# Kernel tuning notes

Measured on AMD Instinct MI355X. Metric: run time of the kernel, lower is better.

The kernel has to match this reference:

```python
import jax, jax.numpy as jnp
import numpy as np

N_NODES = 100000
N_EDGES = 640000
NODE_D = 128   # node_emb_dim == edge_type_emb_dim (required by reverse-net input dim)
MSG_D = 128


def setup_inputs() -> dict:
    key = jax.random.key(0)
    ks = jax.random.split(key, 10)
    cat_d = 3 * NODE_D  # 2*node_emb + edge_type_emb
    s_msg = 1.0 / np.sqrt(cat_d)
    s_upd = 1.0 / np.sqrt(MSG_D)
    return {
        "node_features": jax.random.normal(ks[0], (N_NODES, NODE_D), jnp.float32),
        "edge_features": jax.random.normal(ks[1], (N_EDGES, NODE_D), jnp.float32),
        "from_idx": jax.random.randint(ks[2], (N_EDGES,), 0, N_NODES, jnp.int32),
        "to_idx": jax.random.randint(ks[3], (N_EDGES,), 0, N_NODES, jnp.int32),
        # message net (Linear + ReLU)
        "W_msg": jax.random.uniform(ks[4], (cat_d, MSG_D), jnp.float32, -s_msg, s_msg),
        "b_msg": jnp.zeros((MSG_D,), jnp.float32),
        # reverse message net (separate params)
        "W_rev": jax.random.uniform(ks[5], (cat_d, MSG_D), jnp.float32, -s_msg, s_msg),
        "b_rev": jnp.zeros((MSG_D,), jnp.float32),
        # node-update MLP (Linear + ReLU), residual update
        "W_upd": jax.random.uniform(ks[6], (MSG_D, NODE_D), jnp.float32, -s_upd, s_upd),
        "b_upd": jnp.zeros((NODE_D,), jnp.float32),
    }


def reference(node_features, edge_features, from_idx, to_idx,
              W_msg, b_msg, W_rev, b_rev, W_upd, b_upd):
    # gather endpoints and concat with edge features: [n_edges, 3*node_d]
    edge_inputs = jnp.concatenate(
        [node_features[from_idx], node_features[to_idx], edge_features], axis=-1)
    # forward + reverse message nets (same inputs, different params), summed
    messages = (jax.nn.relu(edge_inputs @ W_msg + b_msg)
                + jax.nn.relu(edge_inputs @ W_rev + b_rev))
    # scatter-sum into destination nodes: [n_nodes, msg_d]
    aggregated = jax.ops.segment_sum(messages, to_idx, num_segments=N_NODES)
    # residual node update: node + MLP(agg)
    return node_features + jax.nn.relu(aggregated @ W_upd + b_upd)
```

## Files before the change

### kernel.cpp

```cpp
#include <hip/hip_runtime.h>
#include <hip/hip_bf16.h>

#define N_NODES 100000
#define N_EDGES 640000

typedef __bf16 bf16_t;
typedef __bf16 bf16x8 __attribute__((ext_vector_type(8)));
typedef float f32x4 __attribute__((ext_vector_type(4)));
typedef float f4 __attribute__((ext_vector_type(4)));
typedef unsigned int u32x4 __attribute__((ext_vector_type(4)));

__device__ __forceinline__ float bflo(unsigned int u) { return __uint_as_float(u << 16); }
__device__ __forceinline__ float bfhi(unsigned int u) { return __uint_as_float(u & 0xffff0000u); }
__device__ __forceinline__ unsigned int bfpack(float a, float b) {
    union { bf16_t h[2]; unsigned int u; } pk;
    pk.h[0] = (bf16_t)a; pk.h[1] = (bf16_t)b;
    return pk.u;
}

__global__ void hist_kernel(const int* __restrict__ to_idx, int* __restrict__ hist) {
    int e = blockIdx.x * 256 + threadIdx.x;
    if (e < N_EDGES) atomicAdd(&hist[to_idx[e]], 1);
}

#define SCAN_CH 1000

__global__ __launch_bounds__(1024)
void scan_reduce_kernel(const int* __restrict__ hist, int* __restrict__ bsum) {
    __shared__ int red[1024];
    int b = blockIdx.x, t = threadIdx.x;
    int v = (t < SCAN_CH) ? hist[b * SCAN_CH + t] : 0;
    red[t] = v;
    __syncthreads();
    for (int off = 512; off > 0; off >>= 1) {
        if (t < off) red[t] += red[t + off];
        __syncthreads();
    }
    if (t == 0) bsum[b] = red[0];
}

__global__ __launch_bounds__(128)
void scan_base_kernel(const int* __restrict__ bsum, int* __restrict__ bbase) {
    __shared__ int s[128];
    int t = threadIdx.x;
    int v = (t < 100) ? bsum[t] : 0;
    s[t] = v;
    __syncthreads();
    for (int off = 1; off < 128; off <<= 1) {
        int u = (t >= off) ? s[t - off] : 0;
        __syncthreads();
        s[t] += u;
        __syncthreads();
    }
    if (t < 100) bbase[t] = s[t] - v;
}

__global__ __launch_bounds__(1024)
void scan_final_kernel(const int* __restrict__ hist,
                       const int* __restrict__ bbase,
                       int* __restrict__ cursor,
                       int* __restrict__ row_start) {
    __shared__ int s[1024];
    int b = blockIdx.x, t = threadIdx.x;
    int v = (t < SCAN_CH) ? hist[b * SCAN_CH + t] : 0;
    s[t] = v;
    __syncthreads();
    for (int off = 1; off < 1024; off <<= 1) {
        int u = (t >= off) ? s[t - off] : 0;
        __syncthreads();
        s[t] += u;
        __syncthreads();
    }
    int excl = bbase[b] + s[t] - v;
    if (t < SCAN_CH) {
        cursor[b * SCAN_CH + t] = excl;
        row_start[b * SCAN_CH + t] = excl;
    }
    if (b == 99 && t == SCAN_CH - 1) row_start[N_NODES] = excl + v;
}

__global__ void inv_scatter_kernel(const int* __restrict__ to_idx,
                                   int* __restrict__ cursor,
                                   int* __restrict__ inv) {
    int e = blockIdx.x * 256 + threadIdx.x;
    if (e < N_EDGES) {
        int pos = atomicAdd(&cursor[to_idx[e]], 1);
        inv[e] = pos;
    }
}

__global__ void prep_w_new(const float* __restrict__ Wmsg,
                           const float* __restrict__ Wrev,
                           const float* __restrict__ Wupd,
                           bf16_t* __restrict__ Wt1,
                           bf16_t* __restrict__ WtE,
                           bf16_t* __restrict__ WtU) {
    int idx = blockIdx.x * 256 + threadIdx.x;
    if (idx < 512 * 128) {
        int p = idx >> 7, k = idx & 127;
        int blk = p >> 7, c = p & 127;
        float v;
        if (blk == 0)      v = Wmsg[k * 128 + c];
        else if (blk == 1) v = Wrev[k * 128 + c];
        else if (blk == 2) v = Wmsg[(128 + k) * 128 + c];
        else               v = Wrev[(128 + k) * 128 + c];
        Wt1[idx] = (bf16_t)v;
    }
    if (idx < 256 * 128) {
        int p = idx >> 7, k = idx & 127;
        float v = (p < 128) ? Wmsg[(256 + k) * 128 + p]
                            : Wrev[(256 + k) * 128 + (p - 128)];
        WtE[idx] = (bf16_t)v;
    }
    if (idx < 128 * 128) {
        int n = idx >> 7, p = idx & 127;
        int colp = 32 * (p >> 5) + ((p >> 1) & 15) + 16 * (p & 1);
        WtU[idx] = (bf16_t)Wupd[colp * 128 + n];
    }
}

__global__ __launch_bounds__(512, 4)
void proj_node_kernel(const float* __restrict__ nodef,
                      const bf16_t* __restrict__ Wt1,
                      unsigned int* __restrict__ A_u) {
    __shared__ char lds_raw[64 * 256];
    const int tid = threadIdx.x;
    const int nb = blockIdx.x * 64;
    const int by = blockIdx.y;

#pragma unroll
    for (int j = 0; j < 4; ++j) {
        int linear = tid + 512 * j;
        int r = linear >> 5, q = linear & 31;
        int node = nb + r;
        f4 v = (f4){0.f, 0.f, 0.f, 0.f};
        if (node < N_NODES)
            v = *reinterpret_cast<const f4*>(nodef + (size_t)node * 128 + q * 4);
        union { bf16_t b[4]; uint2 u; } pk;
        pk.b[0] = (bf16_t)v[0]; pk.b[1] = (bf16_t)v[1];
        pk.b[2] = (bf16_t)v[2]; pk.b[3] = (bf16_t)v[3];
        int byte = (r * 256 + q * 8) ^ ((r & 7) << 4);
        *reinterpret_cast<uint2*>(lds_raw + byte) = pk.u;
    }
    __syncthreads();

    const int wv = tid >> 6;
    const int wr = wv >> 2, wc = wv & 3;
    const int lane = tid & 63;
    const int lhi = lane >> 4, llo = lane & 15;

    f32x4 acc[2][4];
#pragma unroll
    for (int m = 0; m < 2; ++m)
#pragma unroll
        for (int n = 0; n < 4; ++n)
            acc[m][n] = (f32x4){0.f, 0.f, 0.f, 0.f};

    const bf16_t* bptr[4];
#pragma unroll
    for (int n = 0; n < 4; ++n) {
        int colb = (n < 2) ? (wc * 32 + 16 * n) : (128 + wc * 32 + 16 * (n - 2));
        bptr[n] = Wt1 + (size_t)(by * 256 + colb + llo) * 128 + lhi * 8;
    }

#pragma unroll
    for (int k0 = 0; k0 < 4; ++k0) {
        bf16x8 a[2], b[4];
#pragma unroll
        for (int m = 0; m < 2; ++m) {
            int ra = wr * 32 + 16 * m + llo;
            int byte = (ra * 256 + (k0 * 32 + lhi * 8) * 2) ^ ((ra & 7) << 4);
            a[m] = *reinterpret_cast<const bf16x8*>(lds_raw + byte);
        }
#pragma unroll
        for (int n = 0; n < 4; ++n)
            b[n] = *reinterpret_cast<const bf16x8*>(bptr[n] + k0 * 32);
#pragma unroll
        for (int m = 0; m < 2; ++m)
#pragma unroll
            for (int n = 0; n < 4; ++n)
                acc[m][n] = __builtin_amdgcn_mfma_f32_16x16x32_bf16(a[m], b[n], acc[m][n], 0, 0, 0);
    }

    const int wli = wc * 16 + llo;
#pragma unroll
    for (int m = 0; m < 2; ++m) {
        int rbase = wr * 32 + 16 * m + lhi * 4;
#pragma unroll
        for (int r = 0; r < 4; ++r) {
            int node = nb + rbase + r;
            if (node < N_NODES) {
                size_t base = (size_t)node * 256 + by * 128;
                A_u[base + wli]      = bfpack(acc[m][0][r], acc[m][1][r]);
                A_u[base + 64 + wli] = bfpack(acc[m][2][r], acc[m][3][r]);
            }
        }
    }
}

__global__ __launch_bounds__(256, 4)
void edge_fused_kernel(const float* __restrict__ edgef,
                       const int* __restrict__ from_idx,
                       const int* __restrict__ to_idx,
                       const int* __restrict__ inv,
                       const unsigned int* __restrict__ A_u,
                       const bf16_t* __restrict__ WtE,
                       const float* __restrict__ b_msg,
                       const float* __restrict__ b_rev,
                       unsigned int* __restrict__ msgs_u) {
    __shared__ char lds_raw[32 * 256];
    __shared__ int s_from[32], s_dst[32], s_inv[32];

    const int tid = threadIdx.x;
    const int eb = blockIdx.x * 32;

    if (tid < 32) {
        s_from[tid] = from_idx[eb + tid];
        s_dst[tid]  = to_idx[eb + tid];
        s_inv[tid]  = inv[eb + tid];
    }

#pragma unroll
    for (int j = 0; j < 4; ++j) {
        int linear = tid + 256 * j;
        int r = linear >> 5, q = linear & 31;
        f4 v = *reinterpret_cast<const f4*>(edgef + (size_t)(eb + r) * 128 + q * 4);
        union { bf16_t b[4]; uint2 u; } pk;
        pk.b[0] = (bf16_t)v[0]; pk.b[1] = (bf16_t)v[1];
        pk.b[2] = (bf16_t)v[2]; pk.b[3] = (bf16_t)v[3];
        int byte = (r * 256 + q * 8) ^ ((r & 7) << 4);
        *reinterpret_cast<uint2*>(lds_raw + byte) = pk.u;
    }
    __syncthreads();

    const int wc = tid >> 6;
    const int lane = tid & 63;
    const int lhi = lane >> 4, llo = lane & 15;

    f32x4 acc[2][4];
#pragma unroll
    for (int m = 0; m < 2; ++m)
#pragma unroll
        for (int n = 0; n < 4; ++n)
            acc[m][n] = (f32x4){0.f, 0.f, 0.f, 0.f};

    const bf16_t* bptr[4];
#pragma unroll
    for (int n = 0; n < 4; ++n) {
        int colb = (n < 2) ? (wc * 32 + 16 * n) : (128 + wc * 32 + 16 * (n - 2));
        bptr[n] = WtE + (size_t)(colb + llo) * 128 + lhi * 8;
    }

#pragma unroll
    for (int k0 = 0; k0 < 4; ++k0) {
        bf16x8 a[2], b[4];
#pragma unroll
        for (int m = 0; m < 2; ++m) {
            int ra = 16 * m + llo;
            int byte = (ra * 256 + (k0 * 32 + lhi * 8) * 2) ^ ((ra & 7) << 4);
            a[m] = *reinterpret_cast<const bf16x8*>(lds_raw + byte);
        }
#pragma unroll
        for (int n = 0; n < 4; ++n)
            b[n] = *reinterpret_cast<const bf16x8*>(bptr[n] + k0 * 32);
#pragma unroll
        for (int m = 0; m < 2; ++m)
#pragma unroll
            for (int n = 0; n < 4; ++n)
                acc[m][n] = __builtin_amdgcn_mfma_f32_16x16x32_bf16(a[m], b[n], acc[m][n], 0, 0, 0);
    }

    const int wli = wc * 16 + llo;
    unsigned int g[2][4][4];
#pragma unroll
    for (int m = 0; m < 2; ++m) {
#pragma unroll
        for (int r = 0; r < 4; ++r) {
            int rr = 16 * m + lhi * 4 + r;
            const unsigned int* af = A_u + (size_t)s_from[rr] * 256;
            const unsigned int* at = A_u + (size_t)s_dst[rr] * 256 + 128;
            g[m][r][0] = af[wli];
            g[m][r][1] = af[64 + wli];
            g[m][r][2] = at[wli];
            g[m][r][3] = at[64 + wli];
        }
    }

    const int c0 = wc * 32 + llo;
    const float bm0 = b_msg[c0], bm1 = b_msg[c0 + 16];
    const float br0 = b_rev[c0], br1 = b_rev[c0 + 16];
#pragma unroll
    for (int m = 0; m < 2; ++m) {
#pragma unroll
        for (int r = 0; r < 4; ++r) {
            int rr = 16 * m + lhi * 4 + r;
            float m0 = fmaxf(acc[m][0][r] + bm0 + bflo(g[m][r][0]) + bflo(g[m][r][2]), 0.f);
            float m1 = fmaxf(acc[m][1][r] + bm1 + bfhi(g[m][r][0]) + bfhi(g[m][r][2]), 0.f);
            float r0 = fmaxf(acc[m][2][r] + br0 + bflo(g[m][r][1]) + bflo(g[m][r][3]), 0.f);
            float r1 = fmaxf(acc[m][3][r] + br1 + bfhi(g[m][r][1]) + bfhi(g[m][r][3]), 0.f);
            msgs_u[(size_t)s_inv[rr] * 64 + wli] = bfpack(m0 + r0, m1 + r1);
        }
    }
}

__global__ __launch_bounds__(256, 4)
void node_upd_kernel(const unsigned int* __restrict__ msgs_u,
                     const int* __restrict__ row_start,
                     const float* __restrict__ nodef,
                     const bf16_t* __restrict__ WtU,
                     const float* __restrict__ b_upd,
                     float* __restrict__ out) {
    __shared__ char lds_raw[64 * 256];
    __shared__ int s_rs[65];

    const int tid = threadIdx.x;
    const int nb = blockIdx.x * 64;

    if (tid < 65) {
        int nid = nb + tid;
        s_rs[tid] = (nid <= N_NODES) ? row_start[nid] : N_EDGES;
    }
    __syncthreads();

    {
        const int r = tid >> 2;
        const int q = tid & 3;
        float s[32];
#pragma unroll
        for (int i = 0; i < 32; ++i) s[i] = 0.f;
        const int rs = s_rs[r], re = s_rs[r + 1];
        for (int e = rs; e < re; ++e) {
            const u32x4* p = reinterpret_cast<const u32x4*>(msgs_u + (size_t)e * 64 + q * 16);
#pragma unroll
            for (int i = 0; i < 4; ++i) {
                u32x4 w = p[i];
                s[8*i+0] += bflo(w[0]); s[8*i+1] += bfhi(w[0]);
                s[8*i+2] += bflo(w[1]); s[8*i+3] += bfhi(w[1]);
                s[8*i+4] += bflo(w[2]); s[8*i+5] += bfhi(w[2]);
                s[8*i+6] += bflo(w[3]); s[8*i+7] += bfhi(w[3]);
            }
        }
#pragma unroll
        for (int i = 0; i < 4; ++i) {
            union { bf16_t b[8]; u32x4 u; } pk;
#pragma unroll
            for (int w = 0; w < 8; ++w) pk.b[w] = (bf16_t)s[8*i + w];
            int byte = (r * 256 + q * 64 + i * 16) ^ ((r & 7) << 4);
            *reinterpret_cast<u32x4*>(lds_raw + byte) = pk.u;
        }
    }
    __syncthreads();

    const int wv = tid >> 6;
    const int lane = tid & 63;
    const int lhi = lane >> 4, llo = lane & 15;

    f32x4 acc[4][2];
#pragma unroll
    for (int m = 0; m < 4; ++m)
#pragma unroll
        for (int n = 0; n < 2; ++n)
            acc[m][n] = (f32x4){0.f, 0.f, 0.f, 0.f};

#pragma unroll
    for (int k0 = 0; k0 < 4; ++k0) {
        bf16x8 a[4], b[2];
#pragma unroll
        for (int m = 0; m < 4; ++m) {
            int ra = 16 * m + llo;
            int byte = (ra * 256 + (k0 * 32 + lhi * 8) * 2) ^ ((ra & 7) << 4);
            a[m] = *reinterpret_cast<const bf16x8*>(lds_raw + byte);
        }
#pragma unroll
        for (int n = 0; n < 2; ++n) {
            int col = wv * 32 + 16 * n + llo;
            b[n] = *reinterpret_cast<const bf16x8*>(WtU + (size_t)col * 128 + k0 * 32 + lhi * 8);
        }
#pragma unroll
        for (int m = 0; m < 4; ++m)
#pragma unroll
            for (int n = 0; n < 2; ++n)
                acc[m][n] = __builtin_amdgcn_mfma_f32_16x16x32_bf16(a[m], b[n], acc[m][n], 0, 0, 0);
    }

#pragma unroll
    for (int m = 0; m < 4; ++m) {
        int rbase = 16 * m + lhi * 4;
#pragma unroll
        for (int r = 0; r < 4; ++r) {
            int i = nb + rbase + r;
            if (i < N_NODES) {
#pragma unroll
                for (int n = 0; n < 2; ++n) {
                    int c = wv * 32 + 16 * n + llo;
                    out[(size_t)i * 128 + c] =
                        nodef[(size_t)i * 128 + c]
                        + fmaxf(acc[m][n][r] + b_upd[c], 0.f);
                }
            }
        }
    }
}

__global__ __launch_bounds__(256)
void convert_nodef_kernel(const float* __restrict__ nodef,
                          unsigned short* __restrict__ nodef_bf) {
    int i = blockIdx.x * 256 + threadIdx.x;
    if (i < N_NODES * 32) {
        f4 v = *reinterpret_cast<const f4*>(nodef + (size_t)i * 4);
        union { bf16_t b[4]; unsigned long long ll; } pk;
        pk.b[0] = (bf16_t)v[0]; pk.b[1] = (bf16_t)v[1];
        pk.b[2] = (bf16_t)v[2]; pk.b[3] = (bf16_t)v[3];
        *reinterpret_cast<unsigned long long*>(nodef_bf + (size_t)i * 4) = pk.ll;
    }
}

__global__ void prep_w_old(const float* __restrict__ Wmsg,
                           const float* __restrict__ Wrev,
                           const float* __restrict__ Wupd,
                           bf16_t* __restrict__ WtAB,
                           bf16_t* __restrict__ WtU) {
    int idx = blockIdx.x * 256 + threadIdx.x;
    if (idx < 256 * 384) {
        int n = idx / 384;
        int k = idx - n * 384;
        float v = (n < 128) ? Wmsg[k * 128 + n] : Wrev[k * 128 + (n - 128)];
        WtAB[idx] = (bf16_t)v;
    }
    if (idx < 128 * 128) {
        int n = idx >> 7, p = idx & 127;
        int colp = 32 * (p >> 5) + ((p >> 1) & 15) + 16 * (p & 1);
        WtU[idx] = (bf16_t)Wupd[colp * 128 + n];
    }
}

__global__ __launch_bounds__(512, 4)
void edge_msg_old_kernel(const unsigned short* __restrict__ nodef_bf,
                         const float* __restrict__ edgef,
                         const int* __restrict__ from_idx,
                         const int* __restrict__ to_idx,
                         const int* __restrict__ inv,
                         const bf16_t* __restrict__ WtAB,
                         const float* __restrict__ b_msg,
                         const float* __restrict__ b_rev,
                         unsigned int* __restrict__ msgs_u) {
    __shared__ char lds_raw[64 * 384];
    __shared__ int s_from[64], s_dst[64], s_inv[64];

    const int tid = threadIdx.x;
    const int eb = blockIdx.x * 64;

    if (tid < 64) {
        s_from[tid] = from_idx[eb + tid];
        s_dst[tid]  = to_idx[eb + tid];
        s_inv[tid]  = inv[eb + tid];
    }

    const int wv = tid >> 6;
    const int wr = wv >> 2, wc = wv & 3;
    const int lane = tid & 63;
    const int lhi = lane >> 4, llo = lane & 15;

    f32x4 acc[2][4];
#pragma unroll
    for (int m = 0; m < 2; ++m)
#pragma unroll
        for (int n = 0; n < 4; ++n)
            acc[m][n] = (f32x4){0.f, 0.f, 0.f, 0.f};

    const bf16_t* bptr[4];
#pragma unroll
    for (int n = 0; n < 4; ++n) {
        int colb = (n < 2) ? (wc * 32 + 16 * n) : (128 + wc * 32 + 16 * (n - 2));
        bptr[n] = WtAB + (size_t)(colb + llo) * 384 + lhi * 8;
    }

    __syncthreads();

#pragma unroll
    for (int j = 0; j < 3; ++j) {
        int linear = tid + 512 * j;
        int r = linear / 24;
        int q = linear - r * 24;
        const u32x4* src = (q < 16)
            ? reinterpret_cast<const u32x4*>(nodef_bf + (size_t)s_from[r] * 128) + q
            : reinterpret_cast<const u32x4*>(nodef_bf + (size_t)s_dst[r] * 128) + (q - 16);
        u32x4 v = *src;
        int byte = (r * 384 + q * 16) ^ ((r & 7) << 4);
        *reinterpret_cast<u32x4*>(lds_raw + byte) = v;
    }
    __syncthreads();

#pragma unroll
    for (int k0 = 0; k0 < 6; ++k0) {
        bf16x8 a[2], b[4];
#pragma unroll
        for (int m = 0; m < 2; ++m) {
            int ra = wr * 32 + 16 * m + llo;
            int byte = (ra * 384 + k0 * 64 + lhi * 16) ^ ((ra & 7) << 4);
            a[m] = *reinterpret_cast<const bf16x8*>(lds_raw + byte);
        }
#pragma unroll
        for (int n = 0; n < 4; ++n)
            b[n] = *reinterpret_cast<const bf16x8*>(bptr[n] + k0 * 32);
#pragma unroll
        for (int m = 0; m < 2; ++m)
#pragma unroll
            for (int n = 0; n < 4; ++n)
                acc[m][n] = __builtin_amdgcn_mfma_f32_16x16x32_bf16(a[m], b[n], acc[m][n], 0, 0, 0);
    }
    __syncthreads();

#pragma unroll
    for (int j = 0; j < 3; ++j) {
        int linear = tid + 512 * j;
        int r = linear / 24;
        int qq = linear - r * 24;
        u32x4 w;
        if (qq < 8) {
            w = *(reinterpret_cast<const u32x4*>(nodef_bf + (size_t)s_dst[r] * 128) + 8 + qq);
        } else {
            int c = qq - 8;
            const f4* ep = reinterpret_cast<const f4*>(edgef + (size_t)(eb + r) * 128 + c * 8);
            f4 v0 = ep[0];
            f4 v1 = ep[1];
            union { bf16_t b[8]; u32x4 u; } pk;
            pk.b[0] = (bf16_t)v0[0]; pk.b[1] = (bf16_t)v0[1];
            pk.b[2] = (bf16_t)v0[2]; pk.b[3] = (bf16_t)v0[3];
            pk.b[4] = (bf16_t)v1[0]; pk.b[5] = (bf16_t)v1[1];
            pk.b[6] = (bf16_t)v1[2]; pk.b[7] = (bf16_t)v1[3];
            w = pk.u;
        }
        int byte = (r * 384 + qq * 16) ^ ((r & 7) << 4);
        *reinterpret_cast<u32x4*>(lds_raw + byte) = w;
    }
    __syncthreads();

#pragma unroll
    for (int k0 = 0; k0 < 6; ++k0) {
        bf16x8 a[2], b[4];
#pragma unroll
        for (int m = 0; m < 2; ++m) {
            int ra = wr * 32 + 16 * m + llo;
            int byte = (ra * 384 + k0 * 64 + lhi * 16) ^ ((ra & 7) << 4);
            a[m] = *reinterpret_cast<const bf16x8*>(lds_raw + byte);
        }
#pragma unroll
        for (int n = 0; n < 4; ++n)
            b[n] = *reinterpret_cast<const bf16x8*>(bptr[n] + (6 + k0) * 32);
#pragma unroll
        for (int m = 0; m < 2; ++m)
#pragma unroll
            for (int n = 0; n < 4; ++n)
                acc[m][n] = __builtin_amdgcn_mfma_f32_16x16x32_bf16(a[m], b[n], acc[m][n], 0, 0, 0);
    }

    const int c0 = wc * 32 + llo;
    const float bm0 = b_msg[c0], br0 = b_rev[c0];
    const float bm1 = b_msg[c0 + 16], br1 = b_rev[c0 + 16];
#pragma unroll
    for (int m = 0; m < 2; ++m) {
        int rbase = wr * 32 + 16 * m + lhi * 4;
#pragma unroll
        for (int r = 0; r < 4; ++r) {
            float v0 = fmaxf(acc[m][0][r] + bm0, 0.f) + fmaxf(acc[m][2][r] + br0, 0.f);
            float v1 = fmaxf(acc[m][1][r] + bm1, 0.f) + fmaxf(acc[m][3][r] + br1, 0.f);
            msgs_u[(size_t)s_inv[rbase + r] * 64 + wc * 16 + llo] = bfpack(v0, v1);
        }
    }
}

extern "C" void kernel_launch(void* const* d_in, const int* in_sizes, int n_in,
                              void* d_out, int out_size, void* d_ws, size_t ws_size,
                              hipStream_t stream) {
    const float* nodef    = (const float*)d_in[0];
    const float* edgef    = (const float*)d_in[1];
    const int*   from_idx = (const int*)d_in[2];
    const int*   to_idx   = (const int*)d_in[3];
    const float* Wmsg     = (const float*)d_in[4];
    const float* bmsg     = (const float*)d_in[5];
    const float* Wrev     = (const float*)d_in[6];
    const float* brev     = (const float*)d_in[7];
    const float* Wupd     = (const float*)d_in[8];
    const float* bupd     = (const float*)d_in[9];
    float* out = (float*)d_out;
    char* ws = (char*)d_ws;

    if (ws_size >= 271000000) {
        unsigned int* A_u      = (unsigned int*)ws;
        unsigned int* msgs_u   = (unsigned int*)(ws + 102400000);
        bf16_t*       Wt1      = (bf16_t*)(ws + 266240000);
        bf16_t*       WtE      = (bf16_t*)(ws + 266371072);
        bf16_t*       WtU      = (bf16_t*)(ws + 266436608);
        int*          hist     = (int*)(ws + 266469376);
        int*          cursor   = (int*)(ws + 266869376);
        int*          rowstart = (int*)(ws + 267269376);
        int*          inv      = (int*)(ws + 267669392);
        int*          bsum     = (int*)(ws + 270229392);
        int*          bbase    = (int*)(ws + 270229792);

        hipMemsetAsync(hist, 0, (size_t)N_NODES * sizeof(int), stream);
        prep_w_new<<<256, 256, 0, stream>>>(Wmsg, Wrev, Wupd, Wt1, WtE, WtU);
        hist_kernel<<<(N_EDGES + 255) / 256, 256, 0, stream>>>(to_idx, hist);
        scan_reduce_kernel<<<100, 1024, 0, stream>>>(hist, bsum);
        scan_base_kernel<<<1, 128, 0, stream>>>(bsum, bbase);
        scan_final_kernel<<<100, 1024, 0, stream>>>(hist, bbase, cursor, rowstart);
        inv_scatter_kernel<<<(N_EDGES + 255) / 256, 256, 0, stream>>>(to_idx, cursor, inv);
        proj_node_kernel<<<dim3((N_NODES + 63) / 64, 2), 512, 0, stream>>>(nodef, Wt1, A_u);
        edge_fused_kernel<<<N_EDGES / 32, 256, 0, stream>>>(
            edgef, from_idx, to_idx, inv, A_u, WtE, bmsg, brev, msgs_u);
        node_upd_kernel<<<(N_NODES + 63) / 64, 256, 0, stream>>>(
            msgs_u, rowstart, nodef, WtU, bupd, out);
    } else {
        unsigned int*   msgs_u   = (unsigned int*)ws;
        bf16_t*         WtAB     = (bf16_t*)(ws + 163840000);
        bf16_t*         WtU      = (bf16_t*)(ws + 164036608);
        unsigned short* nodef_bf = (unsigned short*)(ws + 164069376);
        int*            hist     = (int*)(ws + 189669376);
        int*            cursor   = (int*)(ws + 190069376);
        int*            rowstart = (int*)(ws + 190469376);
        int*            inv      = (int*)(ws + 190869392);
        int*            bsum     = (int*)(ws + 193429392);
        int*            bbase    = (int*)(ws + 193429792);

        hipMemsetAsync(hist, 0, (size_t)N_NODES * sizeof(int), stream);
        convert_nodef_kernel<<<12500, 256, 0, stream>>>(nodef, nodef_bf);
        prep_w_old<<<384, 256, 0, stream>>>(Wmsg, Wrev, Wupd, WtAB, WtU);
        hist_kernel<<<(N_EDGES + 255) / 256, 256, 0, stream>>>(to_idx, hist);
        scan_reduce_kernel<<<100, 1024, 0, stream>>>(hist, bsum);
        scan_base_kernel<<<1, 128, 0, stream>>>(bsum, bbase);
        scan_final_kernel<<<100, 1024, 0, stream>>>(hist, bbase, cursor, rowstart);
        inv_scatter_kernel<<<(N_EDGES + 255) / 256, 256, 0, stream>>>(to_idx, cursor, inv);
        edge_msg_old_kernel<<<N_EDGES / 64, 512, 0, stream>>>(
            nodef_bf, edgef, from_idx, to_idx, inv, WtAB, bmsg, brev, msgs_u);
        node_upd_kernel<<<(N_NODES + 63) / 64, 256, 0, stream>>>(
            msgs_u, rowstart, nodef, WtU, bupd, out);
    }
}
```

Measured before the change: 461.9 us.

## Interleave node projections for 8-byte gathers, hoist gathers, unroll segment sum

```diff
diff --git a/kernel.cpp b/kernel.cpp
--- a/kernel.cpp
+++ b/kernel.cpp
@@ -191,8 +191,10 @@
             int node = nb + rbase + r;
             if (node < N_NODES) {
                 size_t base = (size_t)node * 256 + by * 128;
-                A_u[base + wli]      = bfpack(acc[m][0][r], acc[m][1][r]);
-                A_u[base + 64 + wli] = bfpack(acc[m][2][r], acc[m][3][r]);
+                uint2 pr;
+                pr.x = bfpack(acc[m][0][r], acc[m][1][r]);
+                pr.y = bfpack(acc[m][2][r], acc[m][3][r]);
+                *reinterpret_cast<uint2*>(A_u + base + 2 * wli) = pr;
             }
         }
     }
@@ -236,6 +238,20 @@
     const int wc = tid >> 6;
     const int lane = tid & 63;
     const int lhi = lane >> 4, llo = lane & 15;
+    const int wli = wc * 16 + llo;
+
+    uint2 gF[2][4], gT[2][4];
+#pragma unroll
+    for (int m = 0; m < 2; ++m) {
+#pragma unroll
+        for (int r = 0; r < 4; ++r) {
+            int rr = 16 * m + lhi * 4 + r;
+            gF[m][r] = *reinterpret_cast<const uint2*>(
+                A_u + (size_t)s_from[rr] * 256 + 2 * wli);
+            gT[m][r] = *reinterpret_cast<const uint2*>(
+                A_u + (size_t)s_dst[rr] * 256 + 128 + 2 * wli);
+        }
+    }
 
     f32x4 acc[2][4];
 #pragma unroll
@@ -270,22 +286,6 @@
                 acc[m][n] = __builtin_amdgcn_mfma_f32_16x16x32_bf16(a[m], b[n], acc[m][n], 0, 0, 0);
     }
 
-    const int wli = wc * 16 + llo;
-    unsigned int g[2][4][4];
-#pragma unroll
-    for (int m = 0; m < 2; ++m) {
-#pragma unroll
-        for (int r = 0; r < 4; ++r) {
-            int rr = 16 * m + lhi * 4 + r;
-            const unsigned int* af = A_u + (size_t)s_from[rr] * 256;
-            const unsigned int* at = A_u + (size_t)s_dst[rr] * 256 + 128;
-            g[m][r][0] = af[wli];
-            g[m][r][1] = af[64 + wli];
-            g[m][r][2] = at[wli];
-            g[m][r][3] = at[64 + wli];
-        }
-    }
-
     const int c0 = wc * 32 + llo;
     const float bm0 = b_msg[c0], bm1 = b_msg[c0 + 16];
     const float br0 = b_rev[c0], br1 = b_rev[c0 + 16];
@@ -294,10 +294,10 @@
 #pragma unroll
         for (int r = 0; r < 4; ++r) {
             int rr = 16 * m + lhi * 4 + r;
-            float m0 = fmaxf(acc[m][0][r] + bm0 + bflo(g[m][r][0]) + bflo(g[m][r][2]), 0.f);
-            float m1 = fmaxf(acc[m][1][r] + bm1 + bfhi(g[m][r][0]) + bfhi(g[m][r][2]), 0.f);
-            float r0 = fmaxf(acc[m][2][r] + br0 + bflo(g[m][r][1]) + bflo(g[m][r][3]), 0.f);
-            float r1 = fmaxf(acc[m][3][r] + br1 + bfhi(g[m][r][1]) + bfhi(g[m][r][3]), 0.f);
+            float m0 = fmaxf(acc[m][0][r] + bm0 + bflo(gF[m][r].x) + bflo(gT[m][r].x), 0.f);
+            float m1 = fmaxf(acc[m][1][r] + bm1 + bfhi(gF[m][r].x) + bfhi(gT[m][r].x), 0.f);
+            float r0 = fmaxf(acc[m][2][r] + br0 + bflo(gF[m][r].y) + bflo(gT[m][r].y), 0.f);
+            float r1 = fmaxf(acc[m][3][r] + br1 + bfhi(gF[m][r].y) + bfhi(gT[m][r].y), 0.f);
             msgs_u[(size_t)s_inv[rr] * 64 + wli] = bfpack(m0 + r0, m1 + r1);
         }
     }
@@ -329,7 +329,26 @@
 #pragma unroll
         for (int i = 0; i < 32; ++i) s[i] = 0.f;
         const int rs = s_rs[r], re = s_rs[r + 1];
-        for (int e = rs; e < re; ++e) {
+        int e = rs;
+        for (; e + 1 < re; e += 2) {
+            const u32x4* p0 = reinterpret_cast<const u32x4*>(msgs_u + (size_t)e * 64 + q * 16);
+            const u32x4* p1 = reinterpret_cast<const u32x4*>(msgs_u + (size_t)(e + 1) * 64 + q * 16);
+            u32x4 w0[4], w1[4];
+#pragma unroll
+            for (int i = 0; i < 4; ++i) { w0[i] = p0[i]; w1[i] = p1[i]; }
+#pragma unroll
+            for (int i = 0; i < 4; ++i) {
+                s[8*i+0] += bflo(w0[i][0]) + bflo(w1[i][0]);
+                s[8*i+1] += bfhi(w0[i][0]) + bfhi(w1[i][0]);
+                s[8*i+2] += bflo(w0[i][1]) + bflo(w1[i][1]);
+                s[8*i+3] += bfhi(w0[i][1]) + bfhi(w1[i][1]);
+                s[8*i+4] += bflo(w0[i][2]) + bflo(w1[i][2]);
+                s[8*i+5] += bfhi(w0[i][2]) + bfhi(w1[i][2]);
+                s[8*i+6] += bflo(w0[i][3]) + bflo(w1[i][3]);
+                s[8*i+7] += bfhi(w0[i][3]) + bfhi(w1[i][3]);
+            }
+        }
+        if (e < re) {
             const u32x4* p = reinterpret_cast<const u32x4*>(msgs_u + (size_t)e * 64 + q * 16);
 #pragma unroll
             for (int i = 0; i < 4; ++i) {
```

Measured after the change: 457.8 us. Within noise of the previous version (-0.9%).
